# Optimization experiments

Hardware: AMD Instinct MI355X
Metric: run time of the kernel (lower is better)

The kernel has to match this reference:

```python
import math
import jax, jax.numpy as jnp
import numpy as np

IN_D = 16
H_DIM = 256
NB_STEPS = 50
B = 8192


def _cc_weights(nb_steps):
    # Clenshaw-Curtis quadrature weights and nodes, exactly as the torch code.
    k = np.arange(0, nb_steps + 1, dtype=np.float64).reshape(-1, 1)
    lam = np.cos(k @ k.T * math.pi / nb_steps)
    lam[:, 0] = 0.5
    lam[:, -1] = 0.5 * lam[:, -1]
    lam = lam * 2.0 / nb_steps
    W = np.arange(0, nb_steps + 1, dtype=np.float64).reshape(-1, 1)
    W[1::2] = 0.0
    W = 2.0 / (1.0 - W ** 2)
    W[0] = 1.0
    W[1::2] = 0.0
    cc = (lam.T @ W).astype(np.float32)  # [nb_steps+1, 1]
    steps = np.cos(np.arange(0, nb_steps + 1) * math.pi / nb_steps).astype(np.float32)  # [nb_steps+1]
    return jnp.asarray(cc), jnp.asarray(steps)


def setup_inputs() -> dict:
    key = jax.random.key(0)
    ks = jax.random.split(key, 16)
    s = 0.05
    return {
        "x": jax.random.normal(ks[0], (B, 1), jnp.float32),
        "h": jax.random.normal(ks[1], (B, IN_D - 1), jnp.float32),
        "iw1": jax.random.normal(ks[2], (H_DIM, IN_D), jnp.float32) * s,
        "ib1": jax.random.normal(ks[3], (H_DIM,), jnp.float32) * s,
        "iw2": jax.random.normal(ks[4], (H_DIM, H_DIM), jnp.float32) * s,
        "ib2": jax.random.normal(ks[5], (H_DIM,), jnp.float32) * s,
        "iw3": jax.random.normal(ks[6], (1, H_DIM), jnp.float32) * s,
        "ib3": jax.random.normal(ks[7], (1,), jnp.float32) * s,
        "nw1": jax.random.normal(ks[8], (H_DIM, IN_D - 1), jnp.float32) * s,
        "nb1": jax.random.normal(ks[9], (H_DIM,), jnp.float32) * s,
        "nw2": jax.random.normal(ks[10], (H_DIM, H_DIM), jnp.float32) * s,
        "nb2": jax.random.normal(ks[11], (H_DIM,), jnp.float32) * s,
        "nw3": jax.random.normal(ks[12], (2, H_DIM), jnp.float32) * s,
        "nb3": jax.random.normal(ks[13], (2,), jnp.float32) * s,
        "nb_steps": NB_STEPS,
    }


def _integrand(z, iw1, ib1, iw2, ib2, iw3, ib3):
    # IntegrandNN: Linear-ReLU-Linear-ReLU-Linear-ELU, then +1.0
    a = jax.nn.relu(z @ iw1.T + ib1)
    a = jax.nn.relu(a @ iw2.T + ib2)
    return jax.nn.elu(a @ iw3.T + ib3) + 1.0


def reference(x, h, iw1, ib1, iw2, ib2, iw3, ib3, nw1, nb1, nw2, nb2, nw3, nb3, nb_steps):
    cc, steps = _cc_weights(int(nb_steps))  # cc: [N+1,1], steps: [N+1]
    Bn, n_pts = x.shape[0], int(nb_steps) + 1
    # x0 = 0, so quadrature nodes X_k = x * (steps_k + 1) / 2 -> [B, N+1, 1]
    X = x[:, None, :] * ((steps[None, :, None] + 1.0) * 0.5)
    Xf = X.reshape(-1, 1)                                             # [B*(N+1), 1]
    Hf = jnp.broadcast_to(h[:, None, :], (Bn, n_pts, h.shape[1])).reshape(-1, h.shape[1])
    z = jnp.concatenate([Xf, Hf], axis=1)                             # [B*(N+1), in_d]
    f = _integrand(z, iw1, ib1, iw2, ib2, iw3, ib3).reshape(Bn, n_pts, 1)
    integral = jnp.sum(f * cc[None, :, :], axis=1) * x * 0.5          # [B, 1]
    # conditioner net on h: Linear-ReLU-Linear-ReLU-Linear -> [B, 2]
    a = jax.nn.relu(h @ nw1.T + nb1)
    a = jax.nn.relu(a @ nw2.T + nb2)
    out = a @ nw3.T + nb3
    offset = out[:, :1]
    scaling = jnp.exp(out[:, 1:2])
    return scaling * integral + offset
```

## Files before the change

kernel.cpp:

```cpp
#include <hip/hip_runtime.h>
#include <hip/hip_bf16.h>
#include <math.h>

#define BATCH 8192
#define HD    256
#define NPTS  51
#define MTOT  (BATCH*NPTS)
#define NTILES 1632

typedef __bf16 bf16x8 __attribute__((ext_vector_type(8)));
typedef float  f32x4  __attribute__((ext_vector_type(4)));

#define OFF_IW2P  0
#define OFF_W1X   131072
#define OFF_CC    132096
#define OFF_STEPS 132352
#define OFF_OFFS  132608
#define OFF_SCAL  165376
#define OFF_G1    198144
#define OFF_FV    8586752

__device__ __forceinline__ unsigned short f2bf(float f) {
    union { float f; unsigned u; } v; v.f = f;
    unsigned r = v.u + 0x7FFFu + ((v.u >> 16) & 1u);
    return (unsigned short)(r >> 16);
}

__device__ __forceinline__ unsigned pk2bf(float lo, float hi) {
    __hip_bfloat162 t = __float22bfloat162_rn(float2{lo, hi});
    union { __hip_bfloat162 b; unsigned u; } v; v.b = t;
    return v.u;
}

__global__ void k1_fused(const float* __restrict__ iw2, const float* __restrict__ nw1,
                         const float* __restrict__ iw1, const float* __restrict__ ib1,
                         const float* __restrict__ nb1, const float* __restrict__ h,
                         const float* __restrict__ nw2, const float* __restrict__ nb2,
                         const float* __restrict__ nw3, const float* __restrict__ nb3,
                         unsigned short* iw2p, float* w1xs, float* cc, float* steps,
                         float* __restrict__ g1, float* __restrict__ offs,
                         float* __restrict__ scal) {
    int blk = blockIdx.x, tid = threadIdx.x;
    if (blk < 256) {
        int t = blk * 256 + tid;
        int n = t >> 8, k = t & 255;
        int half = n >> 7, nl = n & 127, c = k >> 3, j = k & 7;
        iw2p[half * 32768 + c * 1024 + nl * 8 + j] = f2bf(iw2[t]);
    } else if (blk == 256) {
        w1xs[tid] = iw1[tid * 16];
        const float PI_F = 3.14159265358979323846f;
        if (tid <= 50) {
            int j = tid;
            float s = 0.f;
            for (int i = 0; i <= 50; i += 2) {
                float w = (i == 0) ? 1.f : 2.f / (1.f - (float)(i * i));
                float l;
                if (j == 0 || j == 50) l = 0.5f;
                else { int r = (i * j) % 100; l = __cosf((float)r * (PI_F / 50.f)); }
                s += l * w;
            }
            cc[j]    = s * (2.f / 50.f);
            steps[j] = __cosf((float)j * (PI_F / 50.f));
        }
    } else {
        __shared__ float hs[16][15];
        __shared__ unsigned short a1s[16][264];
        __shared__ float Pp[4 * 2 * 16];
        int b0 = (blk - 257) * 16, n = tid;
        if (tid < 240) { int bb = tid / 15, j = tid % 15; hs[bb][j] = h[(b0 + bb) * 15 + j]; }
        __syncthreads();
        float ir[16], nr[15];
        const float4* ip = (const float4*)(iw1 + n * 16);
        ((float4*)ir)[0] = ip[0]; ((float4*)ir)[1] = ip[1];
        ((float4*)ir)[2] = ip[2]; ((float4*)ir)[3] = ip[3];
        #pragma unroll
        for (int j = 0; j < 15; ++j) nr[j] = nw1[n * 15 + j];
        float bi = ib1[n], bn = nb1[n];
        #pragma unroll
        for (int bb = 0; bb < 16; ++bb) {
            float g = bi, a = bn;
            #pragma unroll
            for (int j = 0; j < 15; ++j) { float hv = hs[bb][j]; g += hv * ir[j + 1]; a += hv * nr[j]; }
            g1[(b0 + bb) * 256 + n] = g;
            a1s[bb][n] = f2bf(fmaxf(a, 0.f));
        }
        __syncthreads();

        int lane = tid & 63, w = tid >> 6, l16 = lane & 15, quad = lane >> 4;
        f32x4 acc[4];
        #pragma unroll
        for (int nt = 0; nt < 4; ++nt) acc[nt] = (f32x4){0.f, 0.f, 0.f, 0.f};
        #pragma unroll
        for (int ks = 0; ks < 8; ++ks) {
            bf16x8 af = *(const bf16x8*)&a1s[l16][ks * 32 + quad * 8];
            #pragma unroll
            for (int nt = 0; nt < 4; ++nt) {
                const float* np = nw2 + (w * 64 + nt * 16 + l16) * 256 + ks * 32 + quad * 8;
                float4 f0 = ((const float4*)np)[0];
                float4 f1 = ((const float4*)np)[1];
                union { uint4 u; bf16x8 v; } bf;
                bf.u.x = pk2bf(f0.x, f0.y); bf.u.y = pk2bf(f0.z, f0.w);
                bf.u.z = pk2bf(f1.x, f1.y); bf.u.w = pk2bf(f1.z, f1.w);
                acc[nt] = __builtin_amdgcn_mfma_f32_16x16x32_bf16(af, bf.v, acc[nt], 0, 0, 0);
            }
        }
        float p0[4], p1[4];
        #pragma unroll
        for (int i = 0; i < 4; ++i) { p0[i] = 0.f; p1[i] = 0.f; }
        #pragma unroll
        for (int nt = 0; nt < 4; ++nt) {
            int nn = w * 64 + nt * 16 + l16;
            float bias = nb2[nn], wa = nw3[nn], wb = nw3[256 + nn];
            #pragma unroll
            for (int i = 0; i < 4; ++i) {
                float v = acc[nt][i] + bias;
                v = v > 0.f ? v : 0.f;
                p0[i] += v * wa;
                p1[i] += v * wb;
            }
        }
        #pragma unroll
        for (int mask = 1; mask < 16; mask <<= 1)
            #pragma unroll
            for (int i = 0; i < 4; ++i) {
                p0[i] += __shfl_xor(p0[i], mask, 64);
                p1[i] += __shfl_xor(p1[i], mask, 64);
            }
        if (l16 == 0) {
            #pragma unroll
            for (int i = 0; i < 4; ++i) {
                int r = quad * 4 + i;
                Pp[w * 32 + r]      = p0[i];
                Pp[w * 32 + 16 + r] = p1[i];
            }
        }
        __syncthreads();
        if (tid < 16) {
            float s0 = Pp[tid]      + Pp[32 + tid] + Pp[64 + tid] + Pp[96 + tid]  + nb3[0];
            float s1 = Pp[16 + tid] + Pp[48 + tid] + Pp[80 + tid] + Pp[112 + tid] + nb3[1];
            offs[b0 + tid] = s0;
            scal[b0 + tid] = __expf(s1);
        }
    }
}

__launch_bounds__(512, 2)
__global__ void k2_main(const float* __restrict__ x, const float* __restrict__ g1,
                        const float* __restrict__ w1xs, const unsigned short* __restrict__ iw2p,
                        const float* __restrict__ ib2, const float* __restrict__ iw3,
                        const float* __restrict__ steps,
                        float* __restrict__ fv) {
    __shared__ __align__(16) unsigned char smem[148480];

    int tid = threadIdx.x;
    int lane = tid & 63, w = tid >> 6;
    int l16 = lane & 15, quad = lane >> 4;

    #pragma unroll
    for (int it = 0; it < 16; ++it)
        __builtin_amdgcn_global_load_lds(
            (const __attribute__((address_space(1))) unsigned int*)((const unsigned char*)iw2p + tid * 16 + it * 8192),
            (__attribute__((address_space(3))) unsigned int*)(smem + tid * 16 + it * 8192),
            16, 0, 0);
    if (tid < 64)
        __builtin_amdgcn_global_load_lds(
            (const __attribute__((address_space(1))) unsigned int*)((const unsigned char*)w1xs + tid * 16),
            (__attribute__((address_space(3))) unsigned int*)(smem + 147456 + tid * 16),
            16, 0, 0);
    {
        int m0 = blockIdx.x * 256;
        unsigned blo = (unsigned)(((unsigned long long)(unsigned)m0 * 657931ull) >> 25);
        __builtin_amdgcn_global_load_lds(
            (const __attribute__((address_space(1))) unsigned int*)((const unsigned char*)(g1 + blo * 256) + tid * 16),
            (__attribute__((address_space(3))) unsigned int*)(smem + 131072 + tid * 16),
            16, 0, 0);
    }
    __syncthreads();

    const float* Wl = (const float*)(smem + 147456);

    int p = 0;
    for (int t = blockIdx.x; t < NTILES; t += 256, p ^= 1) {
        int m0 = t * 256;
        unsigned blo = (unsigned)(((unsigned long long)(unsigned)m0 * 657931ull) >> 25);

        if (t + 256 < NTILES) {
            int m0n = (t + 256) * 256;
            unsigned blon = (unsigned)(((unsigned long long)(unsigned)m0n * 657931ull) >> 25);
            __builtin_amdgcn_global_load_lds(
                (const __attribute__((address_space(1))) unsigned int*)((const unsigned char*)(g1 + blon * 256) + tid * 16),
                (__attribute__((address_space(3))) unsigned int*)(smem + 131072 + (p ^ 1) * 8192 + tid * 16),
                16, 0, 0);
        }

        float xs_[2]; int rel_[2];
        #pragma unroll
        for (int mt = 0; mt < 2; ++mt) {
            int m = m0 + w * 32 + mt * 16 + l16;
            unsigned b = (unsigned)(((unsigned long long)(unsigned)m * 657931ull) >> 25);
            int pp = m - (int)b * 51;
            xs_[mt] = x[b] * (steps[pp] + 1.f) * 0.5f;
            rel_[mt] = (int)(b - blo) * 256;
        }
        const float* Ag = (const float*)(smem + 131072 + p * 8192);

        f32x4 acc[2][16];
        #pragma unroll
        for (int mt = 0; mt < 2; ++mt)
            #pragma unroll
            for (int nt = 0; nt < 16; ++nt)
                acc[mt][nt] = (f32x4){0.f, 0.f, 0.f, 0.f};

        #pragma unroll
        for (int ks = 0; ks < 8; ++ks) {
            int ko = ks * 32 + quad * 8;

            union { uint4 u; bf16x8 v; } af[2];
            {
                float4 w0 = ((const float4*)(Wl + ko))[0];
                float4 w1 = ((const float4*)(Wl + ko))[1];
                #pragma unroll
                for (int mt = 0; mt < 2; ++mt) {
                    const float* gp = Ag + rel_[mt] + ko;
                    float4 ga  = ((const float4*)gp)[0];
                    float4 gb2 = ((const float4*)gp)[1];
                    float xs = xs_[mt];
                    float a0 = fmaxf(ga.x  + xs * w0.x, 0.f);
                    float a1 = fmaxf(ga.y  + xs * w0.y, 0.f);
                    float a2 = fmaxf(ga.z  + xs * w0.z, 0.f);
                    float a3 = fmaxf(ga.w  + xs * w0.w, 0.f);
                    float a4 = fmaxf(gb2.x + xs * w1.x, 0.f);
                    float a5 = fmaxf(gb2.y + xs * w1.y, 0.f);
                    float a6 = fmaxf(gb2.z + xs * w1.z, 0.f);
                    float a7 = fmaxf(gb2.w + xs * w1.w, 0.f);
                    af[mt].u.x = pk2bf(a0, a1); af[mt].u.y = pk2bf(a2, a3);
                    af[mt].u.z = pk2bf(a4, a5); af[mt].u.w = pk2bf(a6, a7);
                }
            }

            int cb = (ks * 4 + quad) * 2048 + l16 * 16;
            #pragma unroll
            for (int g = 0; g < 4; ++g) {
                bf16x8 bfr[4];
                #pragma unroll
                for (int nt = 0; nt < 4; ++nt) {
                    int idx = g * 4 + nt;
                    bfr[nt] = *(const bf16x8*)(smem + (idx >> 3) * 65536 + cb + (idx & 7) * 256);
                }
                #pragma unroll
                for (int mt = 0; mt < 2; ++mt)
                    #pragma unroll
                    for (int nt = 0; nt < 4; ++nt)
                        acc[mt][g * 4 + nt] = __builtin_amdgcn_mfma_f32_16x16x32_bf16(
                            af[mt].v, bfr[nt], acc[mt][g * 4 + nt], 0, 0, 0);
            }
        }

        float pf[2][4];
        #pragma unroll
        for (int mt = 0; mt < 2; ++mt)
            #pragma unroll
            for (int i = 0; i < 4; ++i) pf[mt][i] = 0.f;
        #pragma unroll
        for (int idx = 0; idx < 16; ++idx) {
            int n = idx * 16 + l16;
            float bias = ib2[n], w3 = iw3[n];
            #pragma unroll
            for (int mt = 0; mt < 2; ++mt)
                #pragma unroll
                for (int i = 0; i < 4; ++i) {
                    float v = acc[mt][idx][i] + bias;
                    v = v > 0.f ? v : 0.f;
                    pf[mt][i] += v * w3;
                }
        }
        #pragma unroll
        for (int mask = 1; mask < 16; mask <<= 1)
            #pragma unroll
            for (int mt = 0; mt < 2; ++mt)
                #pragma unroll
                for (int i = 0; i < 4; ++i)
                    pf[mt][i] += __shfl_xor(pf[mt][i], mask, 64);
        if (l16 == 0) {
            #pragma unroll
            for (int mt = 0; mt < 2; ++mt)
                #pragma unroll
                for (int i = 0; i < 4; ++i)
                    fv[m0 + w * 32 + mt * 16 + quad * 4 + i] = pf[mt][i];
        }

        __syncthreads();
    }
}

__global__ void k4_final(const float* __restrict__ x, const float* __restrict__ fv,
                         const float* __restrict__ ib3, const float* __restrict__ cc,
                         const float* __restrict__ offs, const float* __restrict__ scal,
                         float* __restrict__ out) {
    int tid = threadIdx.x;
    int wv = tid >> 6, lane = tid & 63;
    int b = blockIdx.x * 4 + wv;
    float v = 0.f;
    if (lane < 51) {
        int m = b * 51 + lane;
        float s = fv[m] + ib3[0];
        float f = s > 0.f ? s + 1.f : __expf(s);
        v = f * cc[lane];
    }
    #pragma unroll
    for (int mask = 1; mask < 64; mask <<= 1) v += __shfl_xor(v, mask, 64);
    if (lane == 0)
        out[b] = scal[b] * (0.5f * x[b] * v) + offs[b];
}

extern "C" void kernel_launch(void* const* d_in, const int* in_sizes, int n_in,
                              void* d_out, int out_size, void* d_ws, size_t ws_size,
                              hipStream_t stream) {
    const float* x   = (const float*)d_in[0];
    const float* h   = (const float*)d_in[1];
    const float* iw1 = (const float*)d_in[2];
    const float* ib1 = (const float*)d_in[3];
    const float* iw2 = (const float*)d_in[4];
    const float* ib2 = (const float*)d_in[5];
    const float* iw3 = (const float*)d_in[6];
    const float* ib3 = (const float*)d_in[7];
    const float* nw1 = (const float*)d_in[8];
    const float* nb1 = (const float*)d_in[9];
    const float* nw2 = (const float*)d_in[10];
    const float* nb2 = (const float*)d_in[11];
    const float* nw3 = (const float*)d_in[12];
    const float* nb3 = (const float*)d_in[13];
    float* out = (float*)d_out;

    char* ws = (char*)d_ws;
    unsigned short* iw2p = (unsigned short*)(ws + OFF_IW2P);
    float* w1xs  = (float*)(ws + OFF_W1X);
    float* cc    = (float*)(ws + OFF_CC);
    float* steps = (float*)(ws + OFF_STEPS);
    float* offs  = (float*)(ws + OFF_OFFS);
    float* scal  = (float*)(ws + OFF_SCAL);
    float* g1    = (float*)(ws + OFF_G1);
    float* fv    = (float*)(ws + OFF_FV);

    k1_fused<<<dim3(769), dim3(256), 0, stream>>>(iw2, nw1, iw1, ib1, nb1, h,
                                                  nw2, nb2, nw3, nb3,
                                                  iw2p, w1xs, cc, steps, g1, offs, scal);
    k2_main<<<dim3(256), dim3(512), 0, stream>>>(x, g1, w1xs, iw2p, ib2, iw3,
                                                 steps, fv);
    k4_final<<<dim3(BATCH / 4), dim3(256), 0, stream>>>(x, fv, ib3, cc, offs, scal, out);
}
```

Baseline: 171.2 us.

## Split warp tiles into 64x128 halves with partial outputs summed in final kernel

Each wave pair now shares a 64-row group, and each wave covers one half of the 256 output columns, so every wave computes a 64x128 tile instead of 32x256. This halves the B-fragment LDS reads per MFMA and lets each wave hoist its ib2/iw3 slices into registers once. In exchange, A-operand construction (relu of g1 plus x*w1) is done four times per wave per k-step. Each column half writes a partial layer-3 dot product to its own buffer, and k4_final adds the two partials before the ELU.

```diff
diff --git a/kernel.cpp b/kernel.cpp
--- a/kernel.cpp
+++ b/kernel.cpp
@@ -18,7 +18,8 @@
 #define OFF_OFFS  132608
 #define OFF_SCAL  165376
 #define OFF_G1    198144
-#define OFF_FV    8586752
+#define OFF_FV0   8586752
+#define OFF_FV1   10257920
 
 __device__ __forceinline__ unsigned short f2bf(float f) {
     union { float f; unsigned u; } v; v.f = f;
@@ -149,11 +150,13 @@
                         const float* __restrict__ w1xs, const unsigned short* __restrict__ iw2p,
                         const float* __restrict__ ib2, const float* __restrict__ iw3,
                         const float* __restrict__ steps,
-                        float* __restrict__ fv) {
+                        float* __restrict__ fv0, float* __restrict__ fv1) {
     __shared__ __align__(16) unsigned char smem[148480];
 
     int tid = threadIdx.x;
     int lane = tid & 63, w = tid >> 6;
+    int rg = w >> 1;
+    int ch = w & 1;
     int l16 = lane & 15, quad = lane >> 4;
 
     #pragma unroll
@@ -178,6 +181,16 @@
     __syncthreads();
 
     const float* Wl = (const float*)(smem + 147456);
+    const unsigned char* Bbase = smem + ch * 65536;
+    float* fvh = ch ? fv1 : fv0;
+
+    float bias_[8], w3_[8];
+    #pragma unroll
+    for (int nt = 0; nt < 8; ++nt) {
+        int n = ch * 128 + nt * 16 + l16;
+        bias_[nt] = ib2[n];
+        w3_[nt]   = iw3[n];
+    }
 
     int p = 0;
     for (int t = blockIdx.x; t < NTILES; t += 256, p ^= 1) {
@@ -193,10 +206,10 @@
                 16, 0, 0);
         }
 
-        float xs_[2]; int rel_[2];
-        #pragma unroll
-        for (int mt = 0; mt < 2; ++mt) {
-            int m = m0 + w * 32 + mt * 16 + l16;
+        float xs_[4]; int rel_[4];
+        #pragma unroll
+        for (int mt = 0; mt < 4; ++mt) {
+            int m = m0 + rg * 64 + mt * 16 + l16;
             unsigned b = (unsigned)(((unsigned long long)(unsigned)m * 657931ull) >> 25);
             int pp = m - (int)b * 51;
             xs_[mt] = x[b] * (steps[pp] + 1.f) * 0.5f;
@@ -204,23 +217,23 @@
         }
         const float* Ag = (const float*)(smem + 131072 + p * 8192);
 
-        f32x4 acc[2][16];
-        #pragma unroll
-        for (int mt = 0; mt < 2; ++mt)
-            #pragma unroll
-            for (int nt = 0; nt < 16; ++nt)
+        f32x4 acc[4][8];
+        #pragma unroll
+        for (int mt = 0; mt < 4; ++mt)
+            #pragma unroll
+            for (int nt = 0; nt < 8; ++nt)
                 acc[mt][nt] = (f32x4){0.f, 0.f, 0.f, 0.f};
 
-        #pragma unroll
+        #pragma unroll 2
         for (int ks = 0; ks < 8; ++ks) {
             int ko = ks * 32 + quad * 8;
 
-            union { uint4 u; bf16x8 v; } af[2];
+            union { uint4 u; bf16x8 v; } af[4];
             {
                 float4 w0 = ((const float4*)(Wl + ko))[0];
                 float4 w1 = ((const float4*)(Wl + ko))[1];
                 #pragma unroll
-                for (int mt = 0; mt < 2; ++mt) {
+                for (int mt = 0; mt < 4; ++mt) {
                     const float* gp = Ag + rel_[mt] + ko;
                     float4 ga  = ((const float4*)gp)[0];
                     float4 gb2 = ((const float4*)gp)[1];
@@ -240,15 +253,13 @@
 
             int cb = (ks * 4 + quad) * 2048 + l16 * 16;
             #pragma unroll
-            for (int g = 0; g < 4; ++g) {
+            for (int g = 0; g < 2; ++g) {
                 bf16x8 bfr[4];
                 #pragma unroll
-                for (int nt = 0; nt < 4; ++nt) {
-                    int idx = g * 4 + nt;
-                    bfr[nt] = *(const bf16x8*)(smem + (idx >> 3) * 65536 + cb + (idx & 7) * 256);
-                }
-                #pragma unroll
-                for (int mt = 0; mt < 2; ++mt)
+                for (int nt = 0; nt < 4; ++nt)
+                    bfr[nt] = *(const bf16x8*)(Bbase + cb + (g * 4 + nt) * 256);
+                #pragma unroll
+                for (int mt = 0; mt < 4; ++mt)
                     #pragma unroll
                     for (int nt = 0; nt < 4; ++nt)
                         acc[mt][g * 4 + nt] = __builtin_amdgcn_mfma_f32_16x16x32_bf16(
@@ -256,20 +267,19 @@
             }
         }
 
-        float pf[2][4];
-        #pragma unroll
-        for (int mt = 0; mt < 2; ++mt)
+        float pf[4][4];
+        #pragma unroll
+        for (int mt = 0; mt < 4; ++mt)
             #pragma unroll
             for (int i = 0; i < 4; ++i) pf[mt][i] = 0.f;
         #pragma unroll
-        for (int idx = 0; idx < 16; ++idx) {
-            int n = idx * 16 + l16;
-            float bias = ib2[n], w3 = iw3[n];
-            #pragma unroll
-            for (int mt = 0; mt < 2; ++mt)
+        for (int nt = 0; nt < 8; ++nt) {
+            float bias = bias_[nt], w3 = w3_[nt];
+            #pragma unroll
+            for (int mt = 0; mt < 4; ++mt)
                 #pragma unroll
                 for (int i = 0; i < 4; ++i) {
-                    float v = acc[mt][idx][i] + bias;
+                    float v = acc[mt][nt][i] + bias;
                     v = v > 0.f ? v : 0.f;
                     pf[mt][i] += v * w3;
                 }
@@ -277,24 +287,25 @@
         #pragma unroll
         for (int mask = 1; mask < 16; mask <<= 1)
             #pragma unroll
-            for (int mt = 0; mt < 2; ++mt)
+            for (int mt = 0; mt < 4; ++mt)
                 #pragma unroll
                 for (int i = 0; i < 4; ++i)
                     pf[mt][i] += __shfl_xor(pf[mt][i], mask, 64);
         if (l16 == 0) {
             #pragma unroll
-            for (int mt = 0; mt < 2; ++mt)
+            for (int mt = 0; mt < 4; ++mt)
                 #pragma unroll
                 for (int i = 0; i < 4; ++i)
-                    fv[m0 + w * 32 + mt * 16 + quad * 4 + i] = pf[mt][i];
+                    fvh[m0 + rg * 64 + mt * 16 + quad * 4 + i] = pf[mt][i];
         }
 
         __syncthreads();
     }
 }
 
-__global__ void k4_final(const float* __restrict__ x, const float* __restrict__ fv,
-                         const float* __restrict__ ib3, const float* __restrict__ cc,
+__global__ void k4_final(const float* __restrict__ x, const float* __restrict__ fv0,
+                         const float* __restrict__ fv1, const float* __restrict__ ib3,
+                         const float* __restrict__ cc,
                          const float* __restrict__ offs, const float* __restrict__ scal,
                          float* __restrict__ out) {
     int tid = threadIdx.x;
@@ -303,7 +314,7 @@
     float v = 0.f;
     if (lane < 51) {
         int m = b * 51 + lane;
-        float s = fv[m] + ib3[0];
+        float s = fv0[m] + fv1[m] + ib3[0];
         float f = s > 0.f ? s + 1.f : __expf(s);
         v = f * cc[lane];
     }
@@ -340,12 +351,13 @@
     float* offs  = (float*)(ws + OFF_OFFS);
     float* scal  = (float*)(ws + OFF_SCAL);
     float* g1    = (float*)(ws + OFF_G1);
-    float* fv    = (float*)(ws + OFF_FV);
+    float* fv0   = (float*)(ws + OFF_FV0);
+    float* fv1   = (float*)(ws + OFF_FV1);
 
     k1_fused<<<dim3(769), dim3(256), 0, stream>>>(iw2, nw1, iw1, ib1, nb1, h,
                                                   nw2, nb2, nw3, nb3,
                                                   iw2p, w1xs, cc, steps, g1, offs, scal);
     k2_main<<<dim3(256), dim3(512), 0, stream>>>(x, g1, w1xs, iw2p, ib2, iw3,
-                                                 steps, fv);
-    k4_final<<<dim3(BATCH / 4), dim3(256), 0, stream>>>(x, fv, ib3, cc, offs, scal, out);
-}
+                                                 steps, fv0, fv1);
+    k4_final<<<dim3(BATCH / 4), dim3(256), 0, stream>>>(x, fv0, fv1, ib3, cc, offs, scal, out);
+}
```

After: 175.6 us. +2.6%, slower.

## Split hidden layer across two blocks per tile and move conditioner net into main kernel

Applied to the files above, without the earlier changes.

The main integrand kernel now splits the 256-wide second hidden layer into two halves handled by separate blocks. Each block stages only half of the packed iw2 weights in LDS, which halves shared memory and accumulator registers so four blocks fit per CU instead of two. The partial layer-3 dot products go to two buffers that the final kernel adds together. The conditioner MLP moves out of the prep kernel into extra blocks of the main launch so it runs alongside the integrand work, at the cost of more global traffic and redundant x/g1 loads across the halves.

```diff
diff --git a/kernel.cpp b/kernel.cpp
--- a/kernel.cpp
+++ b/kernel.cpp
@@ -18,7 +18,8 @@
 #define OFF_OFFS  132608
 #define OFF_SCAL  165376
 #define OFF_G1    198144
-#define OFF_FV    8586752
+#define OFF_FV0   8586752
+#define OFF_FV1   10257920
 
 __device__ __forceinline__ unsigned short f2bf(float f) {
     union { float f; unsigned u; } v; v.f = f;
@@ -32,14 +33,10 @@
     return v.u;
 }
 
-__global__ void k1_fused(const float* __restrict__ iw2, const float* __restrict__ nw1,
-                         const float* __restrict__ iw1, const float* __restrict__ ib1,
-                         const float* __restrict__ nb1, const float* __restrict__ h,
-                         const float* __restrict__ nw2, const float* __restrict__ nb2,
-                         const float* __restrict__ nw3, const float* __restrict__ nb3,
-                         unsigned short* iw2p, float* w1xs, float* cc, float* steps,
-                         float* __restrict__ g1, float* __restrict__ offs,
-                         float* __restrict__ scal) {
+__global__ void k1_prep(const float* __restrict__ iw2, const float* __restrict__ iw1,
+                        const float* __restrict__ ib1, const float* __restrict__ h,
+                        unsigned short* iw2p, float* w1xs, float* cc, float* steps,
+                        float* __restrict__ g1) {
     int blk = blockIdx.x, tid = threadIdx.x;
     if (blk < 256) {
         int t = blk * 256 + tid;
@@ -64,74 +61,109 @@
         }
     } else {
         __shared__ float hs[16][15];
-        __shared__ unsigned short a1s[16][264];
-        __shared__ float Pp[4 * 2 * 16];
         int b0 = (blk - 257) * 16, n = tid;
         if (tid < 240) { int bb = tid / 15, j = tid % 15; hs[bb][j] = h[(b0 + bb) * 15 + j]; }
         __syncthreads();
-        float ir[16], nr[15];
+        float ir[16];
         const float4* ip = (const float4*)(iw1 + n * 16);
         ((float4*)ir)[0] = ip[0]; ((float4*)ir)[1] = ip[1];
         ((float4*)ir)[2] = ip[2]; ((float4*)ir)[3] = ip[3];
-        #pragma unroll
-        for (int j = 0; j < 15; ++j) nr[j] = nw1[n * 15 + j];
-        float bi = ib1[n], bn = nb1[n];
+        float bi = ib1[n];
         #pragma unroll
         for (int bb = 0; bb < 16; ++bb) {
-            float g = bi, a = bn;
-            #pragma unroll
-            for (int j = 0; j < 15; ++j) { float hv = hs[bb][j]; g += hv * ir[j + 1]; a += hv * nr[j]; }
+            float g = bi;
+            #pragma unroll
+            for (int j = 0; j < 15; ++j) g += hs[bb][j] * ir[j + 1];
             g1[(b0 + bb) * 256 + n] = g;
-            a1s[bb][n] = f2bf(fmaxf(a, 0.f));
-        }
-        __syncthreads();
-
-        int lane = tid & 63, w = tid >> 6, l16 = lane & 15, quad = lane >> 4;
-        f32x4 acc[4];
-        #pragma unroll
-        for (int nt = 0; nt < 4; ++nt) acc[nt] = (f32x4){0.f, 0.f, 0.f, 0.f};
-        #pragma unroll
-        for (int ks = 0; ks < 8; ++ks) {
-            bf16x8 af = *(const bf16x8*)&a1s[l16][ks * 32 + quad * 8];
+        }
+    }
+}
+
+__launch_bounds__(512, 4)
+__global__ void k2_main(const float* __restrict__ x, const float* __restrict__ g1,
+                        const float* __restrict__ w1xs, const unsigned short* __restrict__ iw2p,
+                        const float* __restrict__ ib2, const float* __restrict__ iw3,
+                        const float* __restrict__ steps,
+                        const float* __restrict__ h, const float* __restrict__ nw1,
+                        const float* __restrict__ nb1, const float* __restrict__ nw2,
+                        const float* __restrict__ nb2, const float* __restrict__ nw3,
+                        const float* __restrict__ nb3,
+                        float* __restrict__ offs, float* __restrict__ scal,
+                        float* __restrict__ fv0, float* __restrict__ fv1) {
+    __shared__ __align__(16) unsigned char smem[78848];
+    int tid = threadIdx.x, bid = blockIdx.x;
+    int lane = tid & 63, w = tid >> 6;
+    int l16 = lane & 15, quad = lane >> 4;
+
+    if (bid < 512) {
+        float* hs = (float*)smem;
+        unsigned short* a1s = (unsigned short*)(smem + 1024);
+        float* Pp = (float*)(smem + 10240);
+        int b0 = bid * 16;
+        if (tid < 240) { int bb = tid / 15, j = tid % 15; hs[bb * 15 + j] = h[(b0 + bb) * 15 + j]; }
+        __syncthreads();
+        if (tid < 256) {
+            int n = tid;
+            float nr[15];
+            #pragma unroll
+            for (int j = 0; j < 15; ++j) nr[j] = nw1[n * 15 + j];
+            float bn = nb1[n];
+            #pragma unroll
+            for (int bb = 0; bb < 16; ++bb) {
+                float a = bn;
+                #pragma unroll
+                for (int j = 0; j < 15; ++j) a += hs[bb * 15 + j] * nr[j];
+                a1s[bb * 264 + n] = f2bf(fmaxf(a, 0.f));
+            }
+        }
+        __syncthreads();
+        if (tid < 256) {
+            f32x4 acc[4];
+            #pragma unroll
+            for (int nt = 0; nt < 4; ++nt) acc[nt] = (f32x4){0.f, 0.f, 0.f, 0.f};
+            #pragma unroll
+            for (int ks = 0; ks < 8; ++ks) {
+                bf16x8 af = *(const bf16x8*)&a1s[l16 * 264 + ks * 32 + quad * 8];
+                #pragma unroll
+                for (int nt = 0; nt < 4; ++nt) {
+                    const float* np = nw2 + (w * 64 + nt * 16 + l16) * 256 + ks * 32 + quad * 8;
+                    float4 f0 = ((const float4*)np)[0];
+                    float4 f1 = ((const float4*)np)[1];
+                    union { uint4 u; bf16x8 v; } bf;
+                    bf.u.x = pk2bf(f0.x, f0.y); bf.u.y = pk2bf(f0.z, f0.w);
+                    bf.u.z = pk2bf(f1.x, f1.y); bf.u.w = pk2bf(f1.z, f1.w);
+                    acc[nt] = __builtin_amdgcn_mfma_f32_16x16x32_bf16(af, bf.v, acc[nt], 0, 0, 0);
+                }
+            }
+            float p0[4], p1[4];
+            #pragma unroll
+            for (int i = 0; i < 4; ++i) { p0[i] = 0.f; p1[i] = 0.f; }
             #pragma unroll
             for (int nt = 0; nt < 4; ++nt) {
-                const float* np = nw2 + (w * 64 + nt * 16 + l16) * 256 + ks * 32 + quad * 8;
-                float4 f0 = ((const float4*)np)[0];
-                float4 f1 = ((const float4*)np)[1];
-                union { uint4 u; bf16x8 v; } bf;
-                bf.u.x = pk2bf(f0.x, f0.y); bf.u.y = pk2bf(f0.z, f0.w);
-                bf.u.z = pk2bf(f1.x, f1.y); bf.u.w = pk2bf(f1.z, f1.w);
-                acc[nt] = __builtin_amdgcn_mfma_f32_16x16x32_bf16(af, bf.v, acc[nt], 0, 0, 0);
-            }
-        }
-        float p0[4], p1[4];
-        #pragma unroll
-        for (int i = 0; i < 4; ++i) { p0[i] = 0.f; p1[i] = 0.f; }
-        #pragma unroll
-        for (int nt = 0; nt < 4; ++nt) {
-            int nn = w * 64 + nt * 16 + l16;
-            float bias = nb2[nn], wa = nw3[nn], wb = nw3[256 + nn];
-            #pragma unroll
-            for (int i = 0; i < 4; ++i) {
-                float v = acc[nt][i] + bias;
-                v = v > 0.f ? v : 0.f;
-                p0[i] += v * wa;
-                p1[i] += v * wb;
-            }
-        }
-        #pragma unroll
-        for (int mask = 1; mask < 16; mask <<= 1)
-            #pragma unroll
-            for (int i = 0; i < 4; ++i) {
-                p0[i] += __shfl_xor(p0[i], mask, 64);
-                p1[i] += __shfl_xor(p1[i], mask, 64);
-            }
-        if (l16 == 0) {
-            #pragma unroll
-            for (int i = 0; i < 4; ++i) {
-                int r = quad * 4 + i;
-                Pp[w * 32 + r]      = p0[i];
-                Pp[w * 32 + 16 + r] = p1[i];
+                int nn = w * 64 + nt * 16 + l16;
+                float bias = nb2[nn], wa = nw3[nn], wb = nw3[256 + nn];
+                #pragma unroll
+                for (int i = 0; i < 4; ++i) {
+                    float v = acc[nt][i] + bias;
+                    v = v > 0.f ? v : 0.f;
+                    p0[i] += v * wa;
+                    p1[i] += v * wb;
+                }
+            }
+            #pragma unroll
+            for (int mask = 1; mask < 16; mask <<= 1)
+                #pragma unroll
+                for (int i = 0; i < 4; ++i) {
+                    p0[i] += __shfl_xor(p0[i], mask, 64);
+                    p1[i] += __shfl_xor(p1[i], mask, 64);
+                }
+            if (l16 == 0) {
+                #pragma unroll
+                for (int i = 0; i < 4; ++i) {
+                    int r = quad * 4 + i;
+                    Pp[w * 32 + r]      = p0[i];
+                    Pp[w * 32 + 16 + r] = p1[i];
+                }
             }
         }
         __syncthreads();
@@ -141,56 +173,51 @@
             offs[b0 + tid] = s0;
             scal[b0 + tid] = __expf(s1);
         }
-    }
-}
-
-__launch_bounds__(512, 2)
-__global__ void k2_main(const float* __restrict__ x, const float* __restrict__ g1,
-                        const float* __restrict__ w1xs, const unsigned short* __restrict__ iw2p,
-                        const float* __restrict__ ib2, const float* __restrict__ iw3,
-                        const float* __restrict__ steps,
-                        float* __restrict__ fv) {
-    __shared__ __align__(16) unsigned char smem[148480];
-
-    int tid = threadIdx.x;
-    int lane = tid & 63, w = tid >> 6;
-    int l16 = lane & 15, quad = lane >> 4;
+        return;
+    }
+
+    int gb = bid - 512;
+    int ch = gb & 1;
+    int t0 = gb >> 1;
 
     #pragma unroll
-    for (int it = 0; it < 16; ++it)
+    for (int it = 0; it < 8; ++it)
         __builtin_amdgcn_global_load_lds(
-            (const __attribute__((address_space(1))) unsigned int*)((const unsigned char*)iw2p + tid * 16 + it * 8192),
+            (const __attribute__((address_space(1))) unsigned int*)((const unsigned char*)iw2p + ch * 65536 + tid * 16 + it * 8192),
             (__attribute__((address_space(3))) unsigned int*)(smem + tid * 16 + it * 8192),
             16, 0, 0);
     if (tid < 64)
         __builtin_amdgcn_global_load_lds(
             (const __attribute__((address_space(1))) unsigned int*)((const unsigned char*)w1xs + tid * 16),
-            (__attribute__((address_space(3))) unsigned int*)(smem + 147456 + tid * 16),
+            (__attribute__((address_space(3))) unsigned int*)(smem + 77824 + tid * 16),
             16, 0, 0);
     {
-        int m0 = blockIdx.x * 256;
+        int m0 = t0 * 256;
         unsigned blo = (unsigned)(((unsigned long long)(unsigned)m0 * 657931ull) >> 25);
-        __builtin_amdgcn_global_load_lds(
-            (const __attribute__((address_space(1))) unsigned int*)((const unsigned char*)(g1 + blo * 256) + tid * 16),
-            (__attribute__((address_space(3))) unsigned int*)(smem + 131072 + tid * 16),
-            16, 0, 0);
+        if (tid < 384)
+            __builtin_amdgcn_global_load_lds(
+                (const __attribute__((address_space(1))) unsigned int*)((const unsigned char*)(g1 + blo * 256) + tid * 16),
+                (__attribute__((address_space(3))) unsigned int*)(smem + 65536 + tid * 16),
+                16, 0, 0);
     }
     __syncthreads();
 
-    const float* Wl = (const float*)(smem + 147456);
+    const float* Wl = (const float*)(smem + 77824);
+    float* fvh = ch ? fv1 : fv0;
 
     int p = 0;
-    for (int t = blockIdx.x; t < NTILES; t += 256, p ^= 1) {
+    for (int t = t0; t < NTILES; t += 256, p ^= 1) {
         int m0 = t * 256;
         unsigned blo = (unsigned)(((unsigned long long)(unsigned)m0 * 657931ull) >> 25);
 
         if (t + 256 < NTILES) {
             int m0n = (t + 256) * 256;
             unsigned blon = (unsigned)(((unsigned long long)(unsigned)m0n * 657931ull) >> 25);
-            __builtin_amdgcn_global_load_lds(
-                (const __attribute__((address_space(1))) unsigned int*)((const unsigned char*)(g1 + blon * 256) + tid * 16),
-                (__attribute__((address_space(3))) unsigned int*)(smem + 131072 + (p ^ 1) * 8192 + tid * 16),
-                16, 0, 0);
+            if (tid < 384)
+                __builtin_amdgcn_global_load_lds(
+                    (const __attribute__((address_space(1))) unsigned int*)((const unsigned char*)(g1 + blon * 256) + tid * 16),
+                    (__attribute__((address_space(3))) unsigned int*)(smem + 65536 + (p ^ 1) * 6144 + tid * 16),
+                    16, 0, 0);
         }
 
         float xs_[2]; int rel_[2];
@@ -202,16 +229,16 @@
             xs_[mt] = x[b] * (steps[pp] + 1.f) * 0.5f;
             rel_[mt] = (int)(b - blo) * 256;
         }
-        const float* Ag = (const float*)(smem + 131072 + p * 8192);
-
-        f32x4 acc[2][16];
+        const float* Ag = (const float*)(smem + 65536 + p * 6144);
+
+        f32x4 acc[2][8];
         #pragma unroll
         for (int mt = 0; mt < 2; ++mt)
             #pragma unroll
-            for (int nt = 0; nt < 16; ++nt)
+            for (int nt = 0; nt < 8; ++nt)
                 acc[mt][nt] = (f32x4){0.f, 0.f, 0.f, 0.f};
 
-        #pragma unroll
+        #pragma unroll 2
         for (int ks = 0; ks < 8; ++ks) {
             int ko = ks * 32 + quad * 8;
 
@@ -240,13 +267,11 @@
 
             int cb = (ks * 4 + quad) * 2048 + l16 * 16;
             #pragma unroll
-            for (int g = 0; g < 4; ++g) {
+            for (int g = 0; g < 2; ++g) {
                 bf16x8 bfr[4];
                 #pragma unroll
-                for (int nt = 0; nt < 4; ++nt) {
-                    int idx = g * 4 + nt;
-                    bfr[nt] = *(const bf16x8*)(smem + (idx >> 3) * 65536 + cb + (idx & 7) * 256);
-                }
+                for (int nt = 0; nt < 4; ++nt)
+                    bfr[nt] = *(const bf16x8*)(smem + cb + (g * 4 + nt) * 256);
                 #pragma unroll
                 for (int mt = 0; mt < 2; ++mt)
                     #pragma unroll
@@ -262,14 +287,14 @@
             #pragma unroll
             for (int i = 0; i < 4; ++i) pf[mt][i] = 0.f;
         #pragma unroll
-        for (int idx = 0; idx < 16; ++idx) {
-            int n = idx * 16 + l16;
+        for (int nt = 0; nt < 8; ++nt) {
+            int n = ch * 128 + nt * 16 + l16;
             float bias = ib2[n], w3 = iw3[n];
             #pragma unroll
             for (int mt = 0; mt < 2; ++mt)
                 #pragma unroll
                 for (int i = 0; i < 4; ++i) {
-                    float v = acc[mt][idx][i] + bias;
+                    float v = acc[mt][nt][i] + bias;
                     v = v > 0.f ? v : 0.f;
                     pf[mt][i] += v * w3;
                 }
@@ -286,15 +311,16 @@
             for (int mt = 0; mt < 2; ++mt)
                 #pragma unroll
                 for (int i = 0; i < 4; ++i)
-                    fv[m0 + w * 32 + mt * 16 + quad * 4 + i] = pf[mt][i];
-        }
-
-        __syncthreads();
-    }
-}
-
-__global__ void k4_final(const float* __restrict__ x, const float* __restrict__ fv,
-                         const float* __restrict__ ib3, const float* __restrict__ cc,
+                    fvh[m0 + w * 32 + mt * 16 + quad * 4 + i] = pf[mt][i];
+        }
+
+        __syncthreads();
+    }
+}
+
+__global__ void k4_final(const float* __restrict__ x, const float* __restrict__ fv0,
+                         const float* __restrict__ fv1, const float* __restrict__ ib3,
+                         const float* __restrict__ cc,
                          const float* __restrict__ offs, const float* __restrict__ scal,
                          float* __restrict__ out) {
     int tid = threadIdx.x;
@@ -303,7 +329,7 @@
     float v = 0.f;
     if (lane < 51) {
         int m = b * 51 + lane;
-        float s = fv[m] + ib3[0];
+        float s = fv0[m] + fv1[m] + ib3[0];
         float f = s > 0.f ? s + 1.f : __expf(s);
         v = f * cc[lane];
     }
@@ -340,12 +366,13 @@
     float* offs  = (float*)(ws + OFF_OFFS);
     float* scal  = (float*)(ws + OFF_SCAL);
     float* g1    = (float*)(ws + OFF_G1);
-    float* fv    = (float*)(ws + OFF_FV);
-
-    k1_fused<<<dim3(769), dim3(256), 0, stream>>>(iw2, nw1, iw1, ib1, nb1, h,
-                                                  nw2, nb2, nw3, nb3,
-                                                  iw2p, w1xs, cc, steps, g1, offs, scal);
-    k2_main<<<dim3(256), dim3(512), 0, stream>>>(x, g1, w1xs, iw2p, ib2, iw3,
-                                                 steps, fv);
-    k4_final<<<dim3(BATCH / 4), dim3(256), 0, stream>>>(x, fv, ib3, cc, offs, scal, out);
-}
+    float* fv0   = (float*)(ws + OFF_FV0);
+    float* fv1   = (float*)(ws + OFF_FV1);
+
+    k1_prep<<<dim3(769), dim3(256), 0, stream>>>(iw2, iw1, ib1, h,
+                                                 iw2p, w1xs, cc, steps, g1);
+    k2_main<<<dim3(1024), dim3(512), 0, stream>>>(x, g1, w1xs, iw2p, ib2, iw3, steps,
+                                                  h, nw1, nb1, nw2, nb2, nw3, nb3,
+                                                  offs, scal, fv0, fv1);
+    k4_final<<<dim3(BATCH / 4), dim3(256), 0, stream>>>(x, fv0, fv1, ib3, cc, offs, scal, out);
+}
```

Result: faster. 165.1 us (-3.6%).

## Launch one block per tile, split weight load in halves, move conditioner net to final kernel

Applied to the files above, without the earlier changes.

The main kernel switches from a persistent 256-block loop over 1632 tiles to one block per 256-row tile. Each block loads the first half of the packed iw2 into LDS, starts the second half asynchronously, and computes the first half of K while that load is in flight. The cross-lane shuffle reduction is replaced by an LDS transpose-and-sum. The conditioner MLP moves out of the prep kernel into the final reduction kernel, which removes the offs/scal round trip and shortens the prep kernel. The cost is that every block reloads the full 128KB weight matrix instead of amortising it over about six tiles.

```diff
diff --git a/kernel.cpp b/kernel.cpp
--- a/kernel.cpp
+++ b/kernel.cpp
@@ -6,7 +6,6 @@
 #define HD    256
 #define NPTS  51
 #define MTOT  (BATCH*NPTS)
-#define NTILES 1632
 
 typedef __bf16 bf16x8 __attribute__((ext_vector_type(8)));
 typedef float  f32x4  __attribute__((ext_vector_type(4)));
@@ -15,8 +14,6 @@
 #define OFF_W1X   131072
 #define OFF_CC    132096
 #define OFF_STEPS 132352
-#define OFF_OFFS  132608
-#define OFF_SCAL  165376
 #define OFF_G1    198144
 #define OFF_FV    8586752
 
@@ -32,14 +29,10 @@
     return v.u;
 }
 
-__global__ void k1_fused(const float* __restrict__ iw2, const float* __restrict__ nw1,
-                         const float* __restrict__ iw1, const float* __restrict__ ib1,
-                         const float* __restrict__ nb1, const float* __restrict__ h,
-                         const float* __restrict__ nw2, const float* __restrict__ nb2,
-                         const float* __restrict__ nw3, const float* __restrict__ nb3,
-                         unsigned short* iw2p, float* w1xs, float* cc, float* steps,
-                         float* __restrict__ g1, float* __restrict__ offs,
-                         float* __restrict__ scal) {
+__global__ void k1_prep(const float* __restrict__ iw2, const float* __restrict__ iw1,
+                        const float* __restrict__ ib1, const float* __restrict__ h,
+                        unsigned short* iw2p, float* w1xs, float* cc, float* steps,
+                        float* __restrict__ g1) {
     int blk = blockIdx.x, tid = threadIdx.x;
     if (blk < 256) {
         int t = blk * 256 + tid;
@@ -64,29 +57,251 @@
         }
     } else {
         __shared__ float hs[16][15];
-        __shared__ unsigned short a1s[16][264];
-        __shared__ float Pp[4 * 2 * 16];
         int b0 = (blk - 257) * 16, n = tid;
         if (tid < 240) { int bb = tid / 15, j = tid % 15; hs[bb][j] = h[(b0 + bb) * 15 + j]; }
         __syncthreads();
-        float ir[16], nr[15];
+        float ir[16];
         const float4* ip = (const float4*)(iw1 + n * 16);
         ((float4*)ir)[0] = ip[0]; ((float4*)ir)[1] = ip[1];
         ((float4*)ir)[2] = ip[2]; ((float4*)ir)[3] = ip[3];
+        float bi = ib1[n];
+        #pragma unroll
+        for (int bb = 0; bb < 16; ++bb) {
+            float g = bi;
+            #pragma unroll
+            for (int j = 0; j < 15; ++j) g += hs[bb][j] * ir[j + 1];
+            g1[(b0 + bb) * 256 + n] = g;
+        }
+    }
+}
+
+__launch_bounds__(512, 2)
+__global__ void k2_main(const float* __restrict__ x, const float* __restrict__ g1,
+                        const float* __restrict__ w1xs, const unsigned short* __restrict__ iw2p,
+                        const float* __restrict__ ib2, const float* __restrict__ iw3,
+                        const float* __restrict__ steps,
+                        float* __restrict__ fv) {
+    __shared__ __align__(16) unsigned char smem[138240];
+    float* Pp = (float*)smem;
+
+    int tid = threadIdx.x;
+    int m0  = blockIdx.x * 256;
+    int lane = tid & 63, w = tid >> 6;
+    int l16 = lane & 15, quad = lane >> 4;
+
+    unsigned blo = (unsigned)(((unsigned long long)(unsigned)m0 * 657931ull) >> 25);
+
+    const unsigned char* bbase = (const unsigned char*)iw2p;
+
+    #pragma unroll
+    for (int it = 0; it < 8; ++it) {
+        unsigned i = it * 8192 + tid * 16;
+        unsigned a = ((i >> 15) << 16) + (i & 32767);
+        __builtin_amdgcn_global_load_lds(
+            (const __attribute__((address_space(1))) unsigned int*)(bbase + a),
+            (__attribute__((address_space(3))) unsigned int*)(smem + a),
+            16, 0, 0);
+    }
+    if (tid < 384)
+        __builtin_amdgcn_global_load_lds(
+            (const __attribute__((address_space(1))) unsigned int*)((const unsigned char*)(g1 + blo * 256) + tid * 16),
+            (__attribute__((address_space(3))) unsigned int*)(smem + 131072 + tid * 16),
+            16, 0, 0);
+    if (tid < 64)
+        __builtin_amdgcn_global_load_lds(
+            (const __attribute__((address_space(1))) unsigned int*)((const unsigned char*)w1xs + tid * 16),
+            (__attribute__((address_space(3))) unsigned int*)(smem + 137216 + tid * 16),
+            16, 0, 0);
+
+    float xs_[2]; int rel_[2];
+    #pragma unroll
+    for (int mt = 0; mt < 2; ++mt) {
+        int m = m0 + w * 32 + mt * 16 + l16;
+        unsigned b = (unsigned)(((unsigned long long)(unsigned)m * 657931ull) >> 25);
+        int p = m - (int)b * 51;
+        xs_[mt] = x[b] * (steps[p] + 1.f) * 0.5f;
+        rel_[mt] = (int)(b - blo) * 256;
+    }
+
+    f32x4 acc[2][16];
+    #pragma unroll
+    for (int mt = 0; mt < 2; ++mt)
+        #pragma unroll
+        for (int nt = 0; nt < 16; ++nt)
+            acc[mt][nt] = (f32x4){0.f, 0.f, 0.f, 0.f};
+
+    const float* Ag = (const float*)(smem + 131072);
+    const float* Wl = (const float*)(smem + 137216);
+
+    __syncthreads();
+
+    #pragma unroll
+    for (int it = 0; it < 8; ++it) {
+        unsigned i = it * 8192 + tid * 16;
+        unsigned a = ((i >> 15) << 16) + 32768 + (i & 32767);
+        __builtin_amdgcn_global_load_lds(
+            (const __attribute__((address_space(1))) unsigned int*)(bbase + a),
+            (__attribute__((address_space(3))) unsigned int*)(smem + a),
+            16, 0, 0);
+    }
+
+    #pragma unroll 2
+    for (int ks = 0; ks < 4; ++ks) {
+        int ko = ks * 32 + quad * 8;
+        union { uint4 u; bf16x8 v; } af[2];
+        {
+            float4 w0 = ((const float4*)(Wl + ko))[0];
+            float4 w1 = ((const float4*)(Wl + ko))[1];
+            #pragma unroll
+            for (int mt = 0; mt < 2; ++mt) {
+                const float* gp = Ag + rel_[mt] + ko;
+                float4 ga  = ((const float4*)gp)[0];
+                float4 gb2 = ((const float4*)gp)[1];
+                float xs = xs_[mt];
+                float a0 = fmaxf(ga.x  + xs * w0.x, 0.f);
+                float a1 = fmaxf(ga.y  + xs * w0.y, 0.f);
+                float a2 = fmaxf(ga.z  + xs * w0.z, 0.f);
+                float a3 = fmaxf(ga.w  + xs * w0.w, 0.f);
+                float a4 = fmaxf(gb2.x + xs * w1.x, 0.f);
+                float a5 = fmaxf(gb2.y + xs * w1.y, 0.f);
+                float a6 = fmaxf(gb2.z + xs * w1.z, 0.f);
+                float a7 = fmaxf(gb2.w + xs * w1.w, 0.f);
+                af[mt].u.x = pk2bf(a0, a1); af[mt].u.y = pk2bf(a2, a3);
+                af[mt].u.z = pk2bf(a4, a5); af[mt].u.w = pk2bf(a6, a7);
+            }
+        }
+        int cb = (ks * 4 + quad) * 2048 + l16 * 16;
+        #pragma unroll
+        for (int g = 0; g < 4; ++g) {
+            bf16x8 bfr[4];
+            #pragma unroll
+            for (int nt = 0; nt < 4; ++nt) {
+                int idx = g * 4 + nt;
+                bfr[nt] = *(const bf16x8*)(smem + (idx >> 3) * 65536 + cb + (idx & 7) * 256);
+            }
+            #pragma unroll
+            for (int mt = 0; mt < 2; ++mt)
+                #pragma unroll
+                for (int nt = 0; nt < 4; ++nt)
+                    acc[mt][g * 4 + nt] = __builtin_amdgcn_mfma_f32_16x16x32_bf16(
+                        af[mt].v, bfr[nt], acc[mt][g * 4 + nt], 0, 0, 0);
+        }
+    }
+
+    __syncthreads();
+
+    #pragma unroll 2
+    for (int ks = 4; ks < 8; ++ks) {
+        int ko = ks * 32 + quad * 8;
+        union { uint4 u; bf16x8 v; } af[2];
+        {
+            float4 w0 = ((const float4*)(Wl + ko))[0];
+            float4 w1 = ((const float4*)(Wl + ko))[1];
+            #pragma unroll
+            for (int mt = 0; mt < 2; ++mt) {
+                const float* gp = Ag + rel_[mt] + ko;
+                float4 ga  = ((const float4*)gp)[0];
+                float4 gb2 = ((const float4*)gp)[1];
+                float xs = xs_[mt];
+                float a0 = fmaxf(ga.x  + xs * w0.x, 0.f);
+                float a1 = fmaxf(ga.y  + xs * w0.y, 0.f);
+                float a2 = fmaxf(ga.z  + xs * w0.z, 0.f);
+                float a3 = fmaxf(ga.w  + xs * w0.w, 0.f);
+                float a4 = fmaxf(gb2.x + xs * w1.x, 0.f);
+                float a5 = fmaxf(gb2.y + xs * w1.y, 0.f);
+                float a6 = fmaxf(gb2.z + xs * w1.z, 0.f);
+                float a7 = fmaxf(gb2.w + xs * w1.w, 0.f);
+                af[mt].u.x = pk2bf(a0, a1); af[mt].u.y = pk2bf(a2, a3);
+                af[mt].u.z = pk2bf(a4, a5); af[mt].u.w = pk2bf(a6, a7);
+            }
+        }
+        int cb = (ks * 4 + quad) * 2048 + l16 * 16;
+        #pragma unroll
+        for (int g = 0; g < 4; ++g) {
+            bf16x8 bfr[4];
+            #pragma unroll
+            for (int nt = 0; nt < 4; ++nt) {
+                int idx = g * 4 + nt;
+                bfr[nt] = *(const bf16x8*)(smem + (idx >> 3) * 65536 + cb + (idx & 7) * 256);
+            }
+            #pragma unroll
+            for (int mt = 0; mt < 2; ++mt)
+                #pragma unroll
+                for (int nt = 0; nt < 4; ++nt)
+                    acc[mt][g * 4 + nt] = __builtin_amdgcn_mfma_f32_16x16x32_bf16(
+                        af[mt].v, bfr[nt], acc[mt][g * 4 + nt], 0, 0, 0);
+        }
+    }
+
+    float pf[2][4];
+    #pragma unroll
+    for (int mt = 0; mt < 2; ++mt)
+        #pragma unroll
+        for (int i = 0; i < 4; ++i) pf[mt][i] = 0.f;
+    #pragma unroll
+    for (int idx = 0; idx < 16; ++idx) {
+        int n = idx * 16 + l16;
+        float bias = ib2[n], w3 = iw3[n];
+        #pragma unroll
+        for (int mt = 0; mt < 2; ++mt)
+            #pragma unroll
+            for (int i = 0; i < 4; ++i) {
+                float v = acc[mt][idx][i] + bias;
+                v = v > 0.f ? v : 0.f;
+                pf[mt][i] += v * w3;
+            }
+    }
+    __syncthreads();
+    #pragma unroll
+    for (int mt = 0; mt < 2; ++mt)
+        #pragma unroll
+        for (int i = 0; i < 4; ++i) {
+            int row = w * 32 + mt * 16 + quad * 4 + i;
+            Pp[row * 20 + l16] = pf[mt][i];
+        }
+    __syncthreads();
+    if (tid < 256) {
+        const float4* pp = (const float4*)(Pp + tid * 20);
+        float4 v0 = pp[0], v1 = pp[1], v2 = pp[2], v3 = pp[3];
+        float s = v0.x + v0.y + v0.z + v0.w + v1.x + v1.y + v1.z + v1.w
+                + v2.x + v2.y + v2.z + v2.w + v3.x + v3.y + v3.z + v3.w;
+        fv[m0 + tid] = s;
+    }
+}
+
+__global__ void k4_final(const float* __restrict__ x, const float* __restrict__ fv,
+                         const float* __restrict__ ib3, const float* __restrict__ cc,
+                         const float* __restrict__ h, const float* __restrict__ nw1,
+                         const float* __restrict__ nb1, const float* __restrict__ nw2,
+                         const float* __restrict__ nb2, const float* __restrict__ nw3,
+                         const float* __restrict__ nb3,
+                         float* __restrict__ out) {
+    __shared__ float hs[16][15];
+    __shared__ unsigned short a1s[16][264];
+    __shared__ float Pp[128];
+    __shared__ float offsL[16], scalL[16];
+    int tid = threadIdx.x;
+    int lane = tid & 63, w = tid >> 6, l16 = lane & 15, quad = lane >> 4;
+    int b0 = blockIdx.x * 16;
+
+    if (tid < 240) { int bb = tid / 15, j = tid % 15; hs[bb][j] = h[(b0 + bb) * 15 + j]; }
+    __syncthreads();
+    {
+        int n = tid;
+        float nr[15];
         #pragma unroll
         for (int j = 0; j < 15; ++j) nr[j] = nw1[n * 15 + j];
-        float bi = ib1[n], bn = nb1[n];
+        float bn = nb1[n];
         #pragma unroll
         for (int bb = 0; bb < 16; ++bb) {
-            float g = bi, a = bn;
-            #pragma unroll
-            for (int j = 0; j < 15; ++j) { float hv = hs[bb][j]; g += hv * ir[j + 1]; a += hv * nr[j]; }
-            g1[(b0 + bb) * 256 + n] = g;
+            float a = bn;
+            #pragma unroll
+            for (int j = 0; j < 15; ++j) a += hs[bb][j] * nr[j];
             a1s[bb][n] = f2bf(fmaxf(a, 0.f));
         }
-        __syncthreads();
-
-        int lane = tid & 63, w = tid >> 6, l16 = lane & 15, quad = lane >> 4;
+    }
+    __syncthreads();
+    {
         f32x4 acc[4];
         #pragma unroll
         for (int nt = 0; nt < 4; ++nt) acc[nt] = (f32x4){0.f, 0.f, 0.f, 0.f};
@@ -134,183 +349,33 @@
                 Pp[w * 32 + 16 + r] = p1[i];
             }
         }
-        __syncthreads();
-        if (tid < 16) {
-            float s0 = Pp[tid]      + Pp[32 + tid] + Pp[64 + tid] + Pp[96 + tid]  + nb3[0];
-            float s1 = Pp[16 + tid] + Pp[48 + tid] + Pp[80 + tid] + Pp[112 + tid] + nb3[1];
-            offs[b0 + tid] = s0;
-            scal[b0 + tid] = __expf(s1);
-        }
-    }
-}
-
-__launch_bounds__(512, 2)
-__global__ void k2_main(const float* __restrict__ x, const float* __restrict__ g1,
-                        const float* __restrict__ w1xs, const unsigned short* __restrict__ iw2p,
-                        const float* __restrict__ ib2, const float* __restrict__ iw3,
-                        const float* __restrict__ steps,
-                        float* __restrict__ fv) {
-    __shared__ __align__(16) unsigned char smem[148480];
-
-    int tid = threadIdx.x;
-    int lane = tid & 63, w = tid >> 6;
-    int l16 = lane & 15, quad = lane >> 4;
-
-    #pragma unroll
-    for (int it = 0; it < 16; ++it)
-        __builtin_amdgcn_global_load_lds(
-            (const __attribute__((address_space(1))) unsigned int*)((const unsigned char*)iw2p + tid * 16 + it * 8192),
-            (__attribute__((address_space(3))) unsigned int*)(smem + tid * 16 + it * 8192),
-            16, 0, 0);
-    if (tid < 64)
-        __builtin_amdgcn_global_load_lds(
-            (const __attribute__((address_space(1))) unsigned int*)((const unsigned char*)w1xs + tid * 16),
-            (__attribute__((address_space(3))) unsigned int*)(smem + 147456 + tid * 16),
-            16, 0, 0);
-    {
-        int m0 = blockIdx.x * 256;
-        unsigned blo = (unsigned)(((unsigned long long)(unsigned)m0 * 657931ull) >> 25);
-        __builtin_amdgcn_global_load_lds(
-            (const __attribute__((address_space(1))) unsigned int*)((const unsigned char*)(g1 + blo * 256) + tid * 16),
-            (__attribute__((address_space(3))) unsigned int*)(smem + 131072 + tid * 16),
-            16, 0, 0);
-    }
-    __syncthreads();
-
-    const float* Wl = (const float*)(smem + 147456);
-
-    int p = 0;
-    for (int t = blockIdx.x; t < NTILES; t += 256, p ^= 1) {
-        int m0 = t * 256;
-        unsigned blo = (unsigned)(((unsigned long long)(unsigned)m0 * 657931ull) >> 25);
-
-        if (t + 256 < NTILES) {
-            int m0n = (t + 256) * 256;
-            unsigned blon = (unsigned)(((unsigned long long)(unsigned)m0n * 657931ull) >> 25);
-            __builtin_amdgcn_global_load_lds(
-                (const __attribute__((address_space(1))) unsigned int*)((const unsigned char*)(g1 + blon * 256) + tid * 16),
-                (__attribute__((address_space(3))) unsigned int*)(smem + 131072 + (p ^ 1) * 8192 + tid * 16),
-                16, 0, 0);
-        }
-
-        float xs_[2]; int rel_[2];
-        #pragma unroll
-        for (int mt = 0; mt < 2; ++mt) {
-            int m = m0 + w * 32 + mt * 16 + l16;
-            unsigned b = (unsigned)(((unsigned long long)(unsigned)m * 657931ull) >> 25);
-            int pp = m - (int)b * 51;
-            xs_[mt] = x[b] * (steps[pp] + 1.f) * 0.5f;
-            rel_[mt] = (int)(b - blo) * 256;
-        }
-        const float* Ag = (const float*)(smem + 131072 + p * 8192);
-
-        f32x4 acc[2][16];
-        #pragma unroll
-        for (int mt = 0; mt < 2; ++mt)
-            #pragma unroll
-            for (int nt = 0; nt < 16; ++nt)
-                acc[mt][nt] = (f32x4){0.f, 0.f, 0.f, 0.f};
-
-        #pragma unroll
-        for (int ks = 0; ks < 8; ++ks) {
-            int ko = ks * 32 + quad * 8;
-
-            union { uint4 u; bf16x8 v; } af[2];
-            {
-                float4 w0 = ((const float4*)(Wl + ko))[0];
-                float4 w1 = ((const float4*)(Wl + ko))[1];
-                #pragma unroll
-                for (int mt = 0; mt < 2; ++mt) {
-                    const float* gp = Ag + rel_[mt] + ko;
-                    float4 ga  = ((const float4*)gp)[0];
-                    float4 gb2 = ((const float4*)gp)[1];
-                    float xs = xs_[mt];
-                    float a0 = fmaxf(ga.x  + xs * w0.x, 0.f);
-                    float a1 = fmaxf(ga.y  + xs * w0.y, 0.f);
-                    float a2 = fmaxf(ga.z  + xs * w0.z, 0.f);
-                    float a3 = fmaxf(ga.w  + xs * w0.w, 0.f);
-                    float a4 = fmaxf(gb2.x + xs * w1.x, 0.f);
-                    float a5 = fmaxf(gb2.y + xs * w1.y, 0.f);
-                    float a6 = fmaxf(gb2.z + xs * w1.z, 0.f);
-                    float a7 = fmaxf(gb2.w + xs * w1.w, 0.f);
-                    af[mt].u.x = pk2bf(a0, a1); af[mt].u.y = pk2bf(a2, a3);
-                    af[mt].u.z = pk2bf(a4, a5); af[mt].u.w = pk2bf(a6, a7);
-                }
-            }
-
-            int cb = (ks * 4 + quad) * 2048 + l16 * 16;
-            #pragma unroll
-            for (int g = 0; g < 4; ++g) {
-                bf16x8 bfr[4];
-                #pragma unroll
-                for (int nt = 0; nt < 4; ++nt) {
-                    int idx = g * 4 + nt;
-                    bfr[nt] = *(const bf16x8*)(smem + (idx >> 3) * 65536 + cb + (idx & 7) * 256);
-                }
-                #pragma unroll
-                for (int mt = 0; mt < 2; ++mt)
-                    #pragma unroll
-                    for (int nt = 0; nt < 4; ++nt)
-                        acc[mt][g * 4 + nt] = __builtin_amdgcn_mfma_f32_16x16x32_bf16(
-                            af[mt].v, bfr[nt], acc[mt][g * 4 + nt], 0, 0, 0);
-            }
-        }
-
-        float pf[2][4];
-        #pragma unroll
-        for (int mt = 0; mt < 2; ++mt)
-            #pragma unroll
-            for (int i = 0; i < 4; ++i) pf[mt][i] = 0.f;
-        #pragma unroll
-        for (int idx = 0; idx < 16; ++idx) {
-            int n = idx * 16 + l16;
-            float bias = ib2[n], w3 = iw3[n];
-            #pragma unroll
-            for (int mt = 0; mt < 2; ++mt)
-                #pragma unroll
-                for (int i = 0; i < 4; ++i) {
-                    float v = acc[mt][idx][i] + bias;
-                    v = v > 0.f ? v : 0.f;
-                    pf[mt][i] += v * w3;
-                }
-        }
-        #pragma unroll
-        for (int mask = 1; mask < 16; mask <<= 1)
-            #pragma unroll
-            for (int mt = 0; mt < 2; ++mt)
-                #pragma unroll
-                for (int i = 0; i < 4; ++i)
-                    pf[mt][i] += __shfl_xor(pf[mt][i], mask, 64);
-        if (l16 == 0) {
-            #pragma unroll
-            for (int mt = 0; mt < 2; ++mt)
-                #pragma unroll
-                for (int i = 0; i < 4; ++i)
-                    fv[m0 + w * 32 + mt * 16 + quad * 4 + i] = pf[mt][i];
-        }
-
-        __syncthreads();
-    }
-}
-
-__global__ void k4_final(const float* __restrict__ x, const float* __restrict__ fv,
-                         const float* __restrict__ ib3, const float* __restrict__ cc,
-                         const float* __restrict__ offs, const float* __restrict__ scal,
-                         float* __restrict__ out) {
-    int tid = threadIdx.x;
-    int wv = tid >> 6, lane = tid & 63;
-    int b = blockIdx.x * 4 + wv;
-    float v = 0.f;
-    if (lane < 51) {
-        int m = b * 51 + lane;
-        float s = fv[m] + ib3[0];
-        float f = s > 0.f ? s + 1.f : __expf(s);
-        v = f * cc[lane];
-    }
-    #pragma unroll
-    for (int mask = 1; mask < 64; mask <<= 1) v += __shfl_xor(v, mask, 64);
-    if (lane == 0)
-        out[b] = scal[b] * (0.5f * x[b] * v) + offs[b];
+    }
+    __syncthreads();
+    if (tid < 16) {
+        float s0 = Pp[tid]      + Pp[32 + tid] + Pp[64 + tid] + Pp[96 + tid]  + nb3[0];
+        float s1 = Pp[16 + tid] + Pp[48 + tid] + Pp[80 + tid] + Pp[112 + tid] + nb3[1];
+        offsL[tid] = s0;
+        scalL[tid] = __expf(s1);
+    }
+    __syncthreads();
+
+    float bi3 = ib3[0];
+    #pragma unroll
+    for (int bb = 0; bb < 4; ++bb) {
+        int bl = w * 4 + bb;
+        int b = b0 + bl;
+        float v = 0.f;
+        if (lane < 51) {
+            int m = b * 51 + lane;
+            float s = fv[m] + bi3;
+            float f = s > 0.f ? s + 1.f : __expf(s);
+            v = f * cc[lane];
+        }
+        #pragma unroll
+        for (int mask = 1; mask < 64; mask <<= 1) v += __shfl_xor(v, mask, 64);
+        if (lane == 0)
+            out[b] = scalL[bl] * (0.5f * x[b] * v) + offsL[bl];
+    }
 }
 
 extern "C" void kernel_launch(void* const* d_in, const int* in_sizes, int n_in,
@@ -337,15 +402,13 @@
     float* w1xs  = (float*)(ws + OFF_W1X);
     float* cc    = (float*)(ws + OFF_CC);
     float* steps = (float*)(ws + OFF_STEPS);
-    float* offs  = (float*)(ws + OFF_OFFS);
-    float* scal  = (float*)(ws + OFF_SCAL);
     float* g1    = (float*)(ws + OFF_G1);
     float* fv    = (float*)(ws + OFF_FV);
 
-    k1_fused<<<dim3(769), dim3(256), 0, stream>>>(iw2, nw1, iw1, ib1, nb1, h,
-                                                  nw2, nb2, nw3, nb3,
-                                                  iw2p, w1xs, cc, steps, g1, offs, scal);
-    k2_main<<<dim3(256), dim3(512), 0, stream>>>(x, g1, w1xs, iw2p, ib2, iw3,
-                                                 steps, fv);
-    k4_final<<<dim3(BATCH / 4), dim3(256), 0, stream>>>(x, fv, ib3, cc, offs, scal, out);
-}
+    k1_prep<<<dim3(769), dim3(256), 0, stream>>>(iw2, iw1, ib1, h,
+                                                 iw2p, w1xs, cc, steps, g1);
+    k2_main<<<dim3(MTOT / 256), dim3(512), 0, stream>>>(x, g1, w1xs, iw2p, ib2, iw3,
+                                                        steps, fv);
+    k4_final<<<dim3(BATCH / 16), dim3(256), 0, stream>>>(x, fv, ib3, cc, h,
+                                                         nw1, nb1, nw2, nb2, nw3, nb3, out);
+}
```

After: 170.8 us. About the same (-0.3%).
